# Optimization experiments

Hardware: AMD Instinct MI355X
Metric: run time of the kernel (lower is better)

## Reference

```python
import jax, jax.numpy as jnp
import numpy as np

B, T, D = 4096, 200, 64
NEG_INF = jnp.float32(-2.0**32 + 1)


def setup_inputs() -> dict:
    key = jax.random.key(0)
    ks = jax.random.split(key, 8)
    return {
        "queries": jax.random.normal(ks[0], (B, D), dtype=jnp.float32),
        "keys": jax.random.normal(ks[1], (B, T, D), dtype=jnp.float32),
        "keys_length": jax.random.randint(ks[2], (B,), 0, T, dtype=jnp.int32),
        "W1": jax.random.normal(ks[3], (4 * D, 80), dtype=jnp.float32) * 0.05,
        "b1": jnp.zeros((80,), dtype=jnp.float32),
        "W2": jax.random.normal(ks[4], (80, 40), dtype=jnp.float32) * 0.05,
        "b2": jnp.zeros((40,), dtype=jnp.float32),
        "W3": jax.random.normal(ks[5], (40, 1), dtype=jnp.float32) * 0.05,
        "b3": jnp.zeros((1,), dtype=jnp.float32),
    }


def reference(queries, keys, keys_length, W1, b1, W2, b2, W3, b3):
    # queries: [B, D], keys: [B, T, D], keys_length: [B]
    q = jnp.broadcast_to(queries[:, None, :], keys.shape)  # tile over T
    din_all = jnp.concatenate([q, keys, q - keys, q * keys], axis=-1)  # [B, T, 4D]
    h = jax.nn.sigmoid(din_all @ W1 + b1)
    h = jax.nn.sigmoid(h @ W2 + b2)
    logits = (h @ W3 + b3)[..., 0]  # [B, T]
    # sequence mask: position t valid iff t < keys_length[b]
    mask = jnp.arange(keys.shape[1])[None, :] < keys_length[:, None]
    logits = jnp.where(mask, logits, NEG_INF)
    logits = logits / jnp.sqrt(jnp.float32(keys.shape[-1]))
    attn = jax.nn.softmax(logits, axis=-1)  # [B, T]
    out = jnp.einsum('bt,btd->bd', attn, keys)  # squeeze(matmul([B,1,T],[B,T,D]))
    return out
```

## Files before the change

kernel.cpp:

```cpp
#include <hip/hip_runtime.h>
#include <math.h>

constexpr int B_ = 4096, T_ = 200, D_ = 64, NT = 256;
constexpr float NEG_INF_F = -4294967295.0f;
constexpr float LOG2E = 1.4426950408889634f;

typedef __attribute__((ext_vector_type(8))) __bf16 bf16x8;
typedef __attribute__((ext_vector_type(4))) float f32x4;

__device__ __host__ inline unsigned short f2b_rne(float x) {
    unsigned u = __builtin_bit_cast(unsigned, x);
    u += 0x7FFF + ((u >> 16) & 1);
    return (unsigned short)(u >> 16);
}

__device__ inline unsigned short b16bits(float x) {
    return __builtin_bit_cast(unsigned short, (__bf16)x);
}

__device__ inline float frcp(float x) { return __builtin_amdgcn_rcpf(x); }

__device__ inline float fexp2(float x) {
#if __has_builtin(__builtin_amdgcn_exp2f)
    return __builtin_amdgcn_exp2f(x);
#else
    return exp2f(x);
#endif
}

__device__ inline bf16x8 pack8(float4 lo, float4 hi) {
    bf16x8 r;
    r[0] = (__bf16)lo.x; r[1] = (__bf16)lo.y; r[2] = (__bf16)lo.z; r[3] = (__bf16)lo.w;
    r[4] = (__bf16)hi.x; r[5] = (__bf16)hi.y; r[6] = (__bf16)hi.z; r[7] = (__bf16)hi.w;
    return r;
}

__global__ void fold_weights(const float* __restrict__ W1,
                             const float* __restrict__ W2,
                             unsigned short* __restrict__ w1f,
                             unsigned short* __restrict__ w2f,
                             unsigned short* __restrict__ wqff) {
    int i = blockIdx.x * blockDim.x + threadIdx.x;
    if (i < 10240) {
        int j = i & 7, lane = (i >> 3) & 63, nt = (i >> 9) % 5, s = i / 2560;
        int k = s * 32 + (lane >> 4) * 8 + j;
        int n = nt * 16 + (lane & 15);
        float v = (k < 64) ? W1[(64 + k) * 80 + n] - W1[(128 + k) * 80 + n]
                           : W1[(192 + (k - 64)) * 80 + n];
        w1f[i] = f2b_rne(v * LOG2E);
    } else if (i < 14848) {
        int i2 = i - 10240;
        int j = i2 & 7, lane = (i2 >> 3) & 63, nt = (i2 >> 9) % 3, s = i2 / 1536;
        int k = s * 32 + (lane >> 4) * 8 + j;
        int n = nt * 16 + (lane & 15);
        float v = (k < 80 && n < 40) ? W2[k * 40 + n] * LOG2E : 0.f;
        w2f[i2] = f2b_rne(v);
    } else if (i < 19968) {
        int i3 = i - 14848;
        int j = i3 & 7, lane = (i3 >> 3) & 63, nt = (i3 >> 9) % 5, s = i3 / 2560;
        int d = s * 32 + (lane >> 4) * 8 + j;
        int n = nt * 16 + (lane & 15);
        wqff[i3] = f2b_rne((W1[d * 80 + n] + W1[(128 + d) * 80 + n]) * LOG2E);
    }
}

__global__ __launch_bounds__(NT, 2)
void din_attn(const float* __restrict__ q, const float* __restrict__ keys,
              const int* __restrict__ klen,
              const unsigned short* __restrict__ w1f,
              const unsigned short* __restrict__ w2f,
              const unsigned short* __restrict__ wqff,
              const float* __restrict__ b1, const float* __restrict__ b2,
              const float* __restrict__ W3, const float* __restrict__ b3,
              float* __restrict__ out) {
    const int tid = threadIdx.x;
    const int l = tid & 63, wid = tid >> 6, g4 = l >> 4, ln = l & 15;
    const int b = blockIdx.x * 4 + wid;

    alignas(16) __shared__ unsigned short h1c[4][2][16 * 104];
    __shared__ float red[4][256];

    constexpr float NEGS = NEG_INF_F * (0.125f * LOG2E);

    float* myred = red[wid];
    unsigned short* buf0 = h1c[wid][0];
    unsigned short* buf1 = h1c[wid][1];
    myred[l] = NEGS; myred[64 + l] = NEGS; myred[128 + l] = NEGS;
    myred[192 + l] = (l < 8) ? NEGS : -INFINITY;
    #pragma unroll
    for (int r = 0; r < 4; ++r) {
        buf0[(g4 * 4 + r) * 104 + 80 + ln] = 0;
        buf1[(g4 * 4 + r) * 104 + 80 + ln] = 0;
    }

    const int len = klen[b];
    const int ntile = (len + 15) >> 4;
    const float b3v = b3[0];
    const float* kb = keys + (size_t)b * 200 * 64;

#define LOADK(tile_, B0_, B1_, B2_, B3_) do {                              \
        int t_ = (tile_) * 16 + ln;                                        \
        int tc_ = t_ < 200 ? t_ : 199;                                     \
        const float* row_ = kb + tc_ * 64 + g4 * 8;                        \
        B0_ = *(const float4*)(row_);                                      \
        B1_ = *(const float4*)(row_ + 4);                                  \
        B2_ = *(const float4*)(row_ + 32);                                 \
        B3_ = *(const float4*)(row_ + 36);                                 \
    } while (0)

    if (ntile > 0) {
        float b2v[3], w3v[3];
        #pragma unroll
        for (int nt = 0; nt < 3; ++nt) {
            int idx = nt * 16 + ln;
            b2v[nt] = (idx < 40) ? b2[idx] * LOG2E : 0.f;
            w3v[nt] = (idx < 40) ? W3[idx] : 0.f;
        }

        const float* qb = q + b * 64;
        float4 q0  = *(const float4*)(qb + g4 * 8);
        float4 q0b = *(const float4*)(qb + g4 * 8 + 4);
        float4 q1  = *(const float4*)(qb + 32 + g4 * 8);
        float4 q1b = *(const float4*)(qb + 32 + g4 * 8 + 4);
        bf16x8 qf0 = pack8(q0, q0b);
        bf16x8 qf1 = pack8(q1, q1b);

        float hv[5];
        {
            f32x4 hacc[5];
            #pragma unroll
            for (int nt = 0; nt < 5; ++nt) {
                float bv = b1[nt * 16 + ln] * LOG2E;
                hacc[nt] = (f32x4){bv, bv, bv, bv};
            }
            #pragma unroll
            for (int nt = 0; nt < 5; ++nt) {
                bf16x8 f0 = *(const bf16x8*)&wqff[((0 * 5 + nt) * 64 + l) * 8];
                bf16x8 f1 = *(const bf16x8*)&wqff[((1 * 5 + nt) * 64 + l) * 8];
                hacc[nt] = __builtin_amdgcn_mfma_f32_16x16x32_bf16(qf0, f0, hacc[nt], 0, 0, 0);
                hacc[nt] = __builtin_amdgcn_mfma_f32_16x16x32_bf16(qf1, f1, hacc[nt], 0, 0, 0);
            }
            #pragma unroll
            for (int nt = 0; nt < 5; ++nt) hv[nt] = hacc[nt][0];
        }

        bf16x8 wf_[2][5];
        #pragma unroll
        for (int s = 0; s < 2; ++s) {
            float qa0 = (s == 0) ? q0.x  : q1.x,  qa1 = (s == 0) ? q0.y  : q1.y;
            float qa2 = (s == 0) ? q0.z  : q1.z,  qa3 = (s == 0) ? q0.w  : q1.w;
            float qb0 = (s == 0) ? q0b.x : q1b.x, qb1 = (s == 0) ? q0b.y : q1b.y;
            float qb2 = (s == 0) ? q0b.z : q1b.z, qb3 = (s == 0) ? q0b.w : q1b.w;
            #pragma unroll
            for (int nt = 0; nt < 5; ++nt) {
                bf16x8 wk = *(const bf16x8*)&w1f[((s * 5 + nt) * 64 + l) * 8];
                bf16x8 wq = *(const bf16x8*)&w1f[(((s + 2) * 5 + nt) * 64 + l) * 8];
                bf16x8 r;
                r[0] = (__bf16)fmaf(qa0, (float)wq[0], (float)wk[0]);
                r[1] = (__bf16)fmaf(qa1, (float)wq[1], (float)wk[1]);
                r[2] = (__bf16)fmaf(qa2, (float)wq[2], (float)wk[2]);
                r[3] = (__bf16)fmaf(qa3, (float)wq[3], (float)wk[3]);
                r[4] = (__bf16)fmaf(qb0, (float)wq[4], (float)wk[4]);
                r[5] = (__bf16)fmaf(qb1, (float)wq[5], (float)wk[5]);
                r[6] = (__bf16)fmaf(qb2, (float)wq[6], (float)wk[6]);
                r[7] = (__bf16)fmaf(qb3, (float)wq[7], (float)wk[7]);
                wf_[s][nt] = r;
            }
        }

#define L1SIG(K0_, K1_, K2_, K3_, DST_) do {                               \
        f32x4 acc[5];                                                      \
        _Pragma("unroll")                                                  \
        for (int nt = 0; nt < 5; ++nt)                                     \
            acc[nt] = (f32x4){hv[nt], hv[nt], hv[nt], hv[nt]};             \
        bf16x8 av0 = pack8(K0_, K1_);                                      \
        bf16x8 av1 = pack8(K2_, K3_);                                      \
        _Pragma("unroll")                                                  \
        for (int nt = 0; nt < 5; ++nt) {                                   \
            acc[nt] = __builtin_amdgcn_mfma_f32_16x16x32_bf16(             \
                av0, wf_[0][nt], acc[nt], 0, 0, 0);                        \
            acc[nt] = __builtin_amdgcn_mfma_f32_16x16x32_bf16(             \
                av1, wf_[1][nt], acc[nt], 0, 0, 0);                        \
        }                                                                  \
        _Pragma("unroll")                                                  \
        for (int nt = 0; nt < 5; ++nt)                                     \
            _Pragma("unroll")                                              \
            for (int r = 0; r < 4; ++r) {                                  \
                float sg = frcp(1.f + fexp2(-acc[nt][r]));                 \
                (DST_)[(g4 * 4 + r) * 104 + nt * 16 + ln] = b16bits(sg);   \
            }                                                              \
    } while (0)

#define AFREAD(SRC_) do {                                                  \
        af0 = *(const bf16x8*)((SRC_) + ln * 104 + g4 * 8);                \
        af1 = *(const bf16x8*)((SRC_) + ln * 104 + 32 + g4 * 8);           \
        af2 = *(const bf16x8*)((SRC_) + ln * 104 + 64 + g4 * 8);           \
    } while (0)

#define L2L3(tile_) do {                                                   \
        f32x4 acc2[3];                                                     \
        _Pragma("unroll")                                                  \
        for (int nt = 0; nt < 3; ++nt)                                     \
            acc2[nt] = (f32x4){b2v[nt], b2v[nt], b2v[nt], b2v[nt]};        \
        _Pragma("unroll")                                                  \
        for (int nt = 0; nt < 3; ++nt) {                                   \
            bf16x8 w0_ = *(const bf16x8*)(w2f + ((0 * 3 + nt) * 64 + l) * 8); \
            bf16x8 w1_ = *(const bf16x8*)(w2f + ((1 * 3 + nt) * 64 + l) * 8); \
            bf16x8 w2_ = *(const bf16x8*)(w2f + ((2 * 3 + nt) * 64 + l) * 8); \
            acc2[nt] = __builtin_amdgcn_mfma_f32_16x16x32_bf16(af0, w0_, acc2[nt], 0, 0, 0); \
            acc2[nt] = __builtin_amdgcn_mfma_f32_16x16x32_bf16(af1, w1_, acc2[nt], 0, 0, 0); \
            acc2[nt] = __builtin_amdgcn_mfma_f32_16x16x32_bf16(af2, w2_, acc2[nt], 0, 0, 0); \
        }                                                                  \
        _Pragma("unroll")                                                  \
        for (int r = 0; r < 4; ++r) {                                      \
            float p = w3v[0] * frcp(1.f + fexp2(-acc2[0][r]))              \
                    + w3v[1] * frcp(1.f + fexp2(-acc2[1][r]))              \
                    + w3v[2] * frcp(1.f + fexp2(-acc2[2][r]));             \
            p += __shfl_xor(p, 1); p += __shfl_xor(p, 2);                  \
            p += __shfl_xor(p, 4); p += __shfl_xor(p, 8);                  \
            if (ln == 0) {                                                 \
                int trow = (tile_) * 16 + g4 * 4 + r;                      \
                if (trow < len)                                            \
                    myred[trow] = (p + b3v) * (0.125f * LOG2E);            \
            }                                                              \
        }                                                                  \
    } while (0)

        float4 A0, A1, A2, A3, C0, C1, C2, C3;
        bf16x8 af0, af1, af2;
        LOADK(0, A0, A1, A2, A3);
        L1SIG(A0, A1, A2, A3, buf0);
        if (ntile > 1) {
            LOADK(1, C0, C1, C2, C3);
            int it = 0;
            #pragma unroll 1
            while (it + 2 < ntile) {
                AFREAD(buf0);
                L1SIG(C0, C1, C2, C3, buf1);
                LOADK(it + 2, A0, A1, A2, A3);
                L2L3(it);
                AFREAD(buf1);
                L1SIG(A0, A1, A2, A3, buf0);
                LOADK(it + 3, C0, C1, C2, C3);
                L2L3(it + 1);
                it += 2;
            }
            if (ntile - it == 2) {
                AFREAD(buf0);
                L1SIG(C0, C1, C2, C3, buf1);
                L2L3(it);
                AFREAD(buf1);
                L2L3(it + 1);
            } else {
                AFREAD(buf0);
                L2L3(it);
            }
        } else {
            bf16x8 af0_, af1_, af2_;
            af0_ = af0; af1_ = af1; af2_ = af2;
            AFREAD(buf0);
            L2L3(0);
        }
#undef L1SIG
#undef AFREAD
#undef L2L3
    }

    float v0 = myred[l], v1 = myred[64 + l], v2 = myred[128 + l], v3 = myred[192 + l];
    float m = fmaxf(fmaxf(v0, v1), fmaxf(v2, v3));
    #pragma unroll
    for (int off = 32; off; off >>= 1) m = fmaxf(m, __shfl_xor(m, off));
    float e0 = fexp2(v0 - m), e1 = fexp2(v1 - m);
    float e2 = fexp2(v2 - m), e3 = fexp2(v3 - m);
    float s = (e0 + e1) + (e2 + e3);
    #pragma unroll
    for (int off = 32; off; off >>= 1) s += __shfl_xor(s, off);
    const float is_ = frcp(s);
    myred[l] = e0 * is_; myred[64 + l] = e1 * is_;
    myred[128 + l] = e2 * is_; myred[192 + l] = e3 * is_;

    {
        const int obound = (len == 0) ? 200 : len;
        float4 oq = {0.f, 0.f, 0.f, 0.f};
        #pragma unroll 4
        for (int t = g4; t < obound; t += 4) {
            float w = myred[t];
            float4 kv = *(const float4*)(kb + t * 64 + 4 * ln);
            oq.x = fmaf(w, kv.x, oq.x); oq.y = fmaf(w, kv.y, oq.y);
            oq.z = fmaf(w, kv.z, oq.z); oq.w = fmaf(w, kv.w, oq.w);
        }
        oq.x += __shfl_xor(oq.x, 16); oq.x += __shfl_xor(oq.x, 32);
        oq.y += __shfl_xor(oq.y, 16); oq.y += __shfl_xor(oq.y, 32);
        oq.z += __shfl_xor(oq.z, 16); oq.z += __shfl_xor(oq.z, 32);
        oq.w += __shfl_xor(oq.w, 16); oq.w += __shfl_xor(oq.w, 32);
        if (g4 == 0)
            *(float4*)(out + b * 64 + 4 * ln) = oq;
    }
#undef LOADK
}

extern "C" void kernel_launch(void* const* d_in, const int* in_sizes, int n_in,
                              void* d_out, int out_size, void* d_ws, size_t ws_size,
                              hipStream_t stream) {
    const float* q    = (const float*)d_in[0];
    const float* keys = (const float*)d_in[1];
    const int*   kl   = (const int*)d_in[2];
    const float* W1   = (const float*)d_in[3];
    const float* b1   = (const float*)d_in[4];
    const float* W2   = (const float*)d_in[5];
    const float* b2   = (const float*)d_in[6];
    const float* W3   = (const float*)d_in[7];
    const float* b3   = (const float*)d_in[8];

    unsigned short* w1f  = (unsigned short*)d_ws;
    unsigned short* w2f  = w1f + 10240;
    unsigned short* wqff = w2f + 4608;

    fold_weights<<<(19968 + 255) / 256, 256, 0, stream>>>(W1, W2, w1f, w2f, wqff);
    din_attn<<<B_ / 4, NT, 0, stream>>>(q, keys, kl, w1f, w2f, wqff, b1, b2,
                                        W3, b3, (float*)d_out);
}
```

Measured before the change: 66.12 us.

## Fuse softmax-weighted key accumulation into the MLP tile loop without max subtraction

The final weighted sum over keys now happens inside the tile loop. It reuses the key registers already loaded for the first layer, so the keys are not read from global memory a second time. Softmax is computed without subtracting the max, on the assumption that the logits are small, and the LDS logit buffer goes away. Rows with zero length take an early uniform-average path. The exp without a max shift could overflow for large logits, and the reduction now costs many extra cross-lane shuffles per row.

```diff
diff --git a/kernel.cpp b/kernel.cpp
--- a/kernel.cpp
+++ b/kernel.cpp
@@ -2,7 +2,6 @@
 #include <math.h>
 
 constexpr int B_ = 4096, T_ = 200, D_ = 64, NT = 256;
-constexpr float NEG_INF_F = -4294967295.0f;
 constexpr float LOG2E = 1.4426950408889634f;
 
 typedef __attribute__((ext_vector_type(8))) __bf16 bf16x8;
@@ -78,25 +77,39 @@
     const int b = blockIdx.x * 4 + wid;
 
     alignas(16) __shared__ unsigned short h1c[4][2][16 * 104];
-    __shared__ float red[4][256];
-
-    constexpr float NEGS = NEG_INF_F * (0.125f * LOG2E);
-
-    float* myred = red[wid];
+    __shared__ float olds[4][64];
+
+    const int len = klen[b];
+    const int ntile = (len + 15) >> 4;
+    const float* kb = keys + (size_t)b * 200 * 64;
+
+    if (ntile == 0) {
+        float4 oq = {0.f, 0.f, 0.f, 0.f};
+        #pragma unroll 4
+        for (int t = g4; t < 200; t += 4) {
+            float4 kv = *(const float4*)(kb + t * 64 + 4 * ln);
+            oq.x += kv.x; oq.y += kv.y; oq.z += kv.z; oq.w += kv.w;
+        }
+        oq.x += __shfl_xor(oq.x, 16); oq.x += __shfl_xor(oq.x, 32);
+        oq.y += __shfl_xor(oq.y, 16); oq.y += __shfl_xor(oq.y, 32);
+        oq.z += __shfl_xor(oq.z, 16); oq.z += __shfl_xor(oq.z, 32);
+        oq.w += __shfl_xor(oq.w, 16); oq.w += __shfl_xor(oq.w, 32);
+        if (g4 == 0) {
+            oq.x *= 0.005f; oq.y *= 0.005f; oq.z *= 0.005f; oq.w *= 0.005f;
+            *(float4*)(out + b * 64 + 4 * ln) = oq;
+        }
+        return;
+    }
+
     unsigned short* buf0 = h1c[wid][0];
     unsigned short* buf1 = h1c[wid][1];
-    myred[l] = NEGS; myred[64 + l] = NEGS; myred[128 + l] = NEGS;
-    myred[192 + l] = (l < 8) ? NEGS : -INFINITY;
     #pragma unroll
     for (int r = 0; r < 4; ++r) {
         buf0[(g4 * 4 + r) * 104 + 80 + ln] = 0;
         buf1[(g4 * 4 + r) * 104 + 80 + ln] = 0;
     }
 
-    const int len = klen[b];
-    const int ntile = (len + 15) >> 4;
     const float b3v = b3[0];
-    const float* kb = keys + (size_t)b * 200 * 64;
 
 #define LOADK(tile_, B0_, B1_, B2_, B3_) do {                              \
         int t_ = (tile_) * 16 + ln;                                        \
@@ -108,65 +121,72 @@
         B3_ = *(const float4*)(row_ + 36);                                 \
     } while (0)
 
-    if (ntile > 0) {
-        float b2v[3], w3v[3];
+    float4 A0, A1, A2, A3, C0, C1, C2, C3;
+    LOADK(0, A0, A1, A2, A3);
+    LOADK(1, C0, C1, C2, C3);
+
+    float b2v[3], w3v[3];
+    #pragma unroll
+    for (int nt = 0; nt < 3; ++nt) {
+        int idx = nt * 16 + ln;
+        b2v[nt] = (idx < 40) ? b2[idx] * LOG2E : 0.f;
+        w3v[nt] = (idx < 40) ? W3[idx] : 0.f;
+    }
+
+    const float* qb = q + b * 64;
+    float4 q0  = *(const float4*)(qb + g4 * 8);
+    float4 q0b = *(const float4*)(qb + g4 * 8 + 4);
+    float4 q1  = *(const float4*)(qb + 32 + g4 * 8);
+    float4 q1b = *(const float4*)(qb + 32 + g4 * 8 + 4);
+    bf16x8 qf0 = pack8(q0, q0b);
+    bf16x8 qf1 = pack8(q1, q1b);
+
+    float hv[5];
+    {
+        f32x4 hacc[5];
         #pragma unroll
-        for (int nt = 0; nt < 3; ++nt) {
-            int idx = nt * 16 + ln;
-            b2v[nt] = (idx < 40) ? b2[idx] * LOG2E : 0.f;
-            w3v[nt] = (idx < 40) ? W3[idx] : 0.f;
-        }
-
-        const float* qb = q + b * 64;
-        float4 q0  = *(const float4*)(qb + g4 * 8);
-        float4 q0b = *(const float4*)(qb + g4 * 8 + 4);
-        float4 q1  = *(const float4*)(qb + 32 + g4 * 8);
-        float4 q1b = *(const float4*)(qb + 32 + g4 * 8 + 4);
-        bf16x8 qf0 = pack8(q0, q0b);
-        bf16x8 qf1 = pack8(q1, q1b);
-
-        float hv[5];
-        {
-            f32x4 hacc[5];
-            #pragma unroll
-            for (int nt = 0; nt < 5; ++nt) {
-                float bv = b1[nt * 16 + ln] * LOG2E;
-                hacc[nt] = (f32x4){bv, bv, bv, bv};
-            }
-            #pragma unroll
-            for (int nt = 0; nt < 5; ++nt) {
-                bf16x8 f0 = *(const bf16x8*)&wqff[((0 * 5 + nt) * 64 + l) * 8];
-                bf16x8 f1 = *(const bf16x8*)&wqff[((1 * 5 + nt) * 64 + l) * 8];
-                hacc[nt] = __builtin_amdgcn_mfma_f32_16x16x32_bf16(qf0, f0, hacc[nt], 0, 0, 0);
-                hacc[nt] = __builtin_amdgcn_mfma_f32_16x16x32_bf16(qf1, f1, hacc[nt], 0, 0, 0);
-            }
-            #pragma unroll
-            for (int nt = 0; nt < 5; ++nt) hv[nt] = hacc[nt][0];
-        }
-
-        bf16x8 wf_[2][5];
+        for (int nt = 0; nt < 5; ++nt) {
+            float bv = b1[nt * 16 + ln] * LOG2E;
+            hacc[nt] = (f32x4){bv, bv, bv, bv};
+        }
         #pragma unroll
-        for (int s = 0; s < 2; ++s) {
-            float qa0 = (s == 0) ? q0.x  : q1.x,  qa1 = (s == 0) ? q0.y  : q1.y;
-            float qa2 = (s == 0) ? q0.z  : q1.z,  qa3 = (s == 0) ? q0.w  : q1.w;
-            float qb0 = (s == 0) ? q0b.x : q1b.x, qb1 = (s == 0) ? q0b.y : q1b.y;
-            float qb2 = (s == 0) ? q0b.z : q1b.z, qb3 = (s == 0) ? q0b.w : q1b.w;
-            #pragma unroll
-            for (int nt = 0; nt < 5; ++nt) {
-                bf16x8 wk = *(const bf16x8*)&w1f[((s * 5 + nt) * 64 + l) * 8];
-                bf16x8 wq = *(const bf16x8*)&w1f[(((s + 2) * 5 + nt) * 64 + l) * 8];
-                bf16x8 r;
-                r[0] = (__bf16)fmaf(qa0, (float)wq[0], (float)wk[0]);
-                r[1] = (__bf16)fmaf(qa1, (float)wq[1], (float)wk[1]);
-                r[2] = (__bf16)fmaf(qa2, (float)wq[2], (float)wk[2]);
-                r[3] = (__bf16)fmaf(qa3, (float)wq[3], (float)wk[3]);
-                r[4] = (__bf16)fmaf(qb0, (float)wq[4], (float)wk[4]);
-                r[5] = (__bf16)fmaf(qb1, (float)wq[5], (float)wk[5]);
-                r[6] = (__bf16)fmaf(qb2, (float)wq[6], (float)wk[6]);
-                r[7] = (__bf16)fmaf(qb3, (float)wq[7], (float)wk[7]);
-                wf_[s][nt] = r;
-            }
-        }
+        for (int nt = 0; nt < 5; ++nt) {
+            bf16x8 f0 = *(const bf16x8*)&wqff[((0 * 5 + nt) * 64 + l) * 8];
+            bf16x8 f1 = *(const bf16x8*)&wqff[((1 * 5 + nt) * 64 + l) * 8];
+            hacc[nt] = __builtin_amdgcn_mfma_f32_16x16x32_bf16(qf0, f0, hacc[nt], 0, 0, 0);
+            hacc[nt] = __builtin_amdgcn_mfma_f32_16x16x32_bf16(qf1, f1, hacc[nt], 0, 0, 0);
+        }
+        #pragma unroll
+        for (int nt = 0; nt < 5; ++nt) hv[nt] = hacc[nt][0];
+    }
+
+    bf16x8 wf_[2][5];
+    #pragma unroll
+    for (int s = 0; s < 2; ++s) {
+        float qa0 = (s == 0) ? q0.x  : q1.x,  qa1 = (s == 0) ? q0.y  : q1.y;
+        float qa2 = (s == 0) ? q0.z  : q1.z,  qa3 = (s == 0) ? q0.w  : q1.w;
+        float qb0 = (s == 0) ? q0b.x : q1b.x, qb1 = (s == 0) ? q0b.y : q1b.y;
+        float qb2 = (s == 0) ? q0b.z : q1b.z, qb3 = (s == 0) ? q0b.w : q1b.w;
+        #pragma unroll
+        for (int nt = 0; nt < 5; ++nt) {
+            bf16x8 wk = *(const bf16x8*)&w1f[((s * 5 + nt) * 64 + l) * 8];
+            bf16x8 wq = *(const bf16x8*)&w1f[(((s + 2) * 5 + nt) * 64 + l) * 8];
+            bf16x8 r;
+            r[0] = (__bf16)fmaf(qa0, (float)wq[0], (float)wk[0]);
+            r[1] = (__bf16)fmaf(qa1, (float)wq[1], (float)wk[1]);
+            r[2] = (__bf16)fmaf(qa2, (float)wq[2], (float)wk[2]);
+            r[3] = (__bf16)fmaf(qa3, (float)wq[3], (float)wk[3]);
+            r[4] = (__bf16)fmaf(qb0, (float)wq[4], (float)wk[4]);
+            r[5] = (__bf16)fmaf(qb1, (float)wq[5], (float)wk[5]);
+            r[6] = (__bf16)fmaf(qb2, (float)wq[6], (float)wk[6]);
+            r[7] = (__bf16)fmaf(qb3, (float)wq[7], (float)wk[7]);
+            wf_[s][nt] = r;
+        }
+    }
+
+    float s_part = 0.f;
+    float4 o0 = {0,0,0,0}, o1 = o0, o2 = o0, o3 = o0;
+    float e0_, e1_, e2_, e3_;
 
 #define L1SIG(K0_, K1_, K2_, K3_, DST_) do {                               \
         f32x4 acc[5];                                                      \
@@ -197,7 +217,18 @@
         af2 = *(const bf16x8*)((SRC_) + ln * 104 + 64 + g4 * 8);           \
     } while (0)
 
-#define L2L3(tile_) do {                                                   \
+#define L3E(tile_, r_, ER_) do {                                           \
+        float p_ = w3v[0] * frcp(1.f + fexp2(-acc2[0][r_]))                \
+                 + w3v[1] * frcp(1.f + fexp2(-acc2[1][r_]))                \
+                 + w3v[2] * frcp(1.f + fexp2(-acc2[2][r_]));               \
+        p_ += __shfl_xor(p_, 1); p_ += __shfl_xor(p_, 2);                  \
+        p_ += __shfl_xor(p_, 4); p_ += __shfl_xor(p_, 8);                  \
+        int trow_ = (tile_) * 16 + g4 * 4 + (r_);                          \
+        ER_ = (trow_ < len)                                                \
+            ? fexp2((p_ + b3v) * (0.125f * LOG2E)) : 0.f;                  \
+    } while (0)
+
+#define L2L3E(tile_) do {                                                  \
         f32x4 acc2[3];                                                     \
         _Pragma("unroll")                                                  \
         for (int nt = 0; nt < 3; ++nt)                                     \
@@ -211,92 +242,94 @@
             acc2[nt] = __builtin_amdgcn_mfma_f32_16x16x32_bf16(af1, w1_, acc2[nt], 0, 0, 0); \
             acc2[nt] = __builtin_amdgcn_mfma_f32_16x16x32_bf16(af2, w2_, acc2[nt], 0, 0, 0); \
         }                                                                  \
-        _Pragma("unroll")                                                  \
-        for (int r = 0; r < 4; ++r) {                                      \
-            float p = w3v[0] * frcp(1.f + fexp2(-acc2[0][r]))              \
-                    + w3v[1] * frcp(1.f + fexp2(-acc2[1][r]))              \
-                    + w3v[2] * frcp(1.f + fexp2(-acc2[2][r]));             \
-            p += __shfl_xor(p, 1); p += __shfl_xor(p, 2);                  \
-            p += __shfl_xor(p, 4); p += __shfl_xor(p, 8);                  \
-            if (ln == 0) {                                                 \
-                int trow = (tile_) * 16 + g4 * 4 + r;                      \
-                if (trow < len)                                            \
-                    myred[trow] = (p + b3v) * (0.125f * LOG2E);            \
-            }                                                              \
-        }                                                                  \
-    } while (0)
-
-        float4 A0, A1, A2, A3, C0, C1, C2, C3;
-        bf16x8 af0, af1, af2;
-        LOADK(0, A0, A1, A2, A3);
-        L1SIG(A0, A1, A2, A3, buf0);
-        if (ntile > 1) {
-            LOADK(1, C0, C1, C2, C3);
-            int it = 0;
-            #pragma unroll 1
-            while (it + 2 < ntile) {
-                AFREAD(buf0);
-                L1SIG(C0, C1, C2, C3, buf1);
-                LOADK(it + 2, A0, A1, A2, A3);
-                L2L3(it);
-                AFREAD(buf1);
-                L1SIG(A0, A1, A2, A3, buf0);
-                LOADK(it + 3, C0, C1, C2, C3);
-                L2L3(it + 1);
-                it += 2;
-            }
-            if (ntile - it == 2) {
-                AFREAD(buf0);
-                L1SIG(C0, C1, C2, C3, buf1);
-                L2L3(it);
-                AFREAD(buf1);
-                L2L3(it + 1);
-            } else {
-                AFREAD(buf0);
-                L2L3(it);
-            }
+        L3E(tile_, 0, e0_); L3E(tile_, 1, e1_);                            \
+        L3E(tile_, 2, e2_); L3E(tile_, 3, e3_);                            \
+    } while (0)
+
+#define UPDATE(K0_, K1_, K2_, K3_) do {                                    \
+        s_part += (e0_ + e1_) + (e2_ + e3_);                               \
+        int src_ = (ln >> 2) << 4;                                         \
+        float r0_ = __shfl(e0_, src_), r1_ = __shfl(e1_, src_);            \
+        float r2_ = __shfl(e2_, src_), r3_ = __shfl(e3_, src_);            \
+        int rr_ = ln & 3;                                                  \
+        float pm_ = rr_ == 0 ? r0_ : rr_ == 1 ? r1_ : rr_ == 2 ? r2_ : r3_;\
+        o0.x = fmaf(pm_, K0_.x, o0.x); o0.y = fmaf(pm_, K0_.y, o0.y);      \
+        o0.z = fmaf(pm_, K0_.z, o0.z); o0.w = fmaf(pm_, K0_.w, o0.w);      \
+        o1.x = fmaf(pm_, K1_.x, o1.x); o1.y = fmaf(pm_, K1_.y, o1.y);      \
+        o1.z = fmaf(pm_, K1_.z, o1.z); o1.w = fmaf(pm_, K1_.w, o1.w);      \
+        o2.x = fmaf(pm_, K2_.x, o2.x); o2.y = fmaf(pm_, K2_.y, o2.y);      \
+        o2.z = fmaf(pm_, K2_.z, o2.z); o2.w = fmaf(pm_, K2_.w, o2.w);      \
+        o3.x = fmaf(pm_, K3_.x, o3.x); o3.y = fmaf(pm_, K3_.y, o3.y);      \
+        o3.z = fmaf(pm_, K3_.z, o3.z); o3.w = fmaf(pm_, K3_.w, o3.w);      \
+    } while (0)
+
+    bf16x8 af0, af1, af2;
+    L1SIG(A0, A1, A2, A3, buf0);
+    if (ntile > 1) {
+        int it = 0;
+        #pragma unroll 1
+        while (it + 2 < ntile) {
+            AFREAD(buf0);
+            L1SIG(C0, C1, C2, C3, buf1);
+            L2L3E(it);
+            UPDATE(A0, A1, A2, A3);
+            LOADK(it + 2, A0, A1, A2, A3);
+            AFREAD(buf1);
+            L1SIG(A0, A1, A2, A3, buf0);
+            L2L3E(it + 1);
+            UPDATE(C0, C1, C2, C3);
+            LOADK(it + 3, C0, C1, C2, C3);
+            it += 2;
+        }
+        if (ntile - it == 2) {
+            AFREAD(buf0);
+            L1SIG(C0, C1, C2, C3, buf1);
+            L2L3E(it);
+            UPDATE(A0, A1, A2, A3);
+            AFREAD(buf1);
+            L2L3E(it + 1);
+            UPDATE(C0, C1, C2, C3);
         } else {
-            bf16x8 af0_, af1_, af2_;
-            af0_ = af0; af1_ = af1; af2_ = af2;
             AFREAD(buf0);
-            L2L3(0);
-        }
+            L2L3E(it);
+            UPDATE(A0, A1, A2, A3);
+        }
+    } else {
+        AFREAD(buf0);
+        L2L3E(0);
+        UPDATE(A0, A1, A2, A3);
+    }
+#undef LOADK
 #undef L1SIG
 #undef AFREAD
-#undef L2L3
-    }
-
-    float v0 = myred[l], v1 = myred[64 + l], v2 = myred[128 + l], v3 = myred[192 + l];
-    float m = fmaxf(fmaxf(v0, v1), fmaxf(v2, v3));
-    #pragma unroll
-    for (int off = 32; off; off >>= 1) m = fmaxf(m, __shfl_xor(m, off));
-    float e0 = fexp2(v0 - m), e1 = fexp2(v1 - m);
-    float e2 = fexp2(v2 - m), e3 = fexp2(v3 - m);
-    float s = (e0 + e1) + (e2 + e3);
-    #pragma unroll
-    for (int off = 32; off; off >>= 1) s += __shfl_xor(s, off);
-    const float is_ = frcp(s);
-    myred[l] = e0 * is_; myred[64 + l] = e1 * is_;
-    myred[128 + l] = e2 * is_; myred[192 + l] = e3 * is_;
-
-    {
-        const int obound = (len == 0) ? 200 : len;
-        float4 oq = {0.f, 0.f, 0.f, 0.f};
-        #pragma unroll 4
-        for (int t = g4; t < obound; t += 4) {
-            float w = myred[t];
-            float4 kv = *(const float4*)(kb + t * 64 + 4 * ln);
-            oq.x = fmaf(w, kv.x, oq.x); oq.y = fmaf(w, kv.y, oq.y);
-            oq.z = fmaf(w, kv.z, oq.z); oq.w = fmaf(w, kv.w, oq.w);
-        }
-        oq.x += __shfl_xor(oq.x, 16); oq.x += __shfl_xor(oq.x, 32);
-        oq.y += __shfl_xor(oq.y, 16); oq.y += __shfl_xor(oq.y, 32);
-        oq.z += __shfl_xor(oq.z, 16); oq.z += __shfl_xor(oq.z, 32);
-        oq.w += __shfl_xor(oq.w, 16); oq.w += __shfl_xor(oq.w, 32);
-        if (g4 == 0)
-            *(float4*)(out + b * 64 + 4 * ln) = oq;
-    }
-#undef LOADK
+#undef L3E
+#undef L2L3E
+#undef UPDATE
+
+    float s_tot = s_part;
+    s_tot += __shfl_xor(s_tot, 16);
+    s_tot += __shfl_xor(s_tot, 32);
+    const float inv = frcp(s_tot);
+
+#define RED16(x_) { x_ += __shfl_xor(x_, 1); x_ += __shfl_xor(x_, 2);      \
+                    x_ += __shfl_xor(x_, 4); x_ += __shfl_xor(x_, 8); }
+    RED16(o0.x) RED16(o0.y) RED16(o0.z) RED16(o0.w)
+    RED16(o1.x) RED16(o1.y) RED16(o1.z) RED16(o1.w)
+    RED16(o2.x) RED16(o2.y) RED16(o2.z) RED16(o2.w)
+    RED16(o3.x) RED16(o3.y) RED16(o3.z) RED16(o3.w)
+#undef RED16
+    if (ln == 0) {
+        float* od = olds[wid];
+        od[g4 * 8 + 0] = o0.x; od[g4 * 8 + 1] = o0.y;
+        od[g4 * 8 + 2] = o0.z; od[g4 * 8 + 3] = o0.w;
+        od[g4 * 8 + 4] = o1.x; od[g4 * 8 + 5] = o1.y;
+        od[g4 * 8 + 6] = o1.z; od[g4 * 8 + 7] = o1.w;
+        od[32 + g4 * 8 + 0] = o2.x; od[32 + g4 * 8 + 1] = o2.y;
+        od[32 + g4 * 8 + 2] = o2.z; od[32 + g4 * 8 + 3] = o2.w;
+        od[32 + g4 * 8 + 4] = o3.x; od[32 + g4 * 8 + 5] = o3.y;
+        od[32 + g4 * 8 + 6] = o3.z; od[32 + g4 * 8 + 7] = o3.w;
+    }
+    out[b * 64 + l] = olds[wid][l] * inv;
 }
 
 extern "C" void kernel_launch(void* const* d_in, const int* in_sizes, int n_in,
```

Result: faster. 56.15 us (-15.1%).
